# Performance work log

Measured on AMD Instinct MI355X. Metric: run time of the kernel, lower is better.

## Reference

```python
import jax, jax.numpy as jnp
import numpy as np

B, T, D, H = 8, 4096, 1024, 1024

def setup_inputs() -> dict:
    key = jax.random.key(0)
    k1, k2, k3, k4, k5 = jax.random.split(key, 5)
    s = 1.0 / np.sqrt(D)  # nn.Linear default init scale
    return {
        "x": jax.random.normal(k1, (B, T, D), dtype=jnp.float32),
        "Wz": jax.random.uniform(k2, (H, D), dtype=jnp.float32, minval=-s, maxval=s),
        "bz": jax.random.uniform(k3, (H,), dtype=jnp.float32, minval=-s, maxval=s),
        "Wh": jax.random.uniform(k4, (H, D), dtype=jnp.float32, minval=-s, maxval=s),
        "bh": jax.random.uniform(k5, (H,), dtype=jnp.float32, minval=-s, maxval=s),
    }

def log_g(x):
    # Appendix B.3 of 'Were RNNs All We Needed?'
    return jnp.where(x >= 0, jnp.log(jax.nn.relu(x) + 0.5), -jax.nn.softplus(-x))

def reference(x, Wz, bz, Wh, bh):
    # Linear projections: [B,T,D] @ [D,H] -> [B,T,H]
    k = jnp.einsum('btd,hd->bth', x, Wz) + bz
    tilde_h = jnp.einsum('btd,hd->bth', x, Wh) + bh
    log_z = -jax.nn.softplus(-k)           # log sigmoid(k)
    log_one_minus_z = -jax.nn.softplus(k)  # log (1 - sigmoid(k))
    log_tilde_h = log_g(tilde_h)
    # parallel scan in log space: h[i] = a[i]*h[i-1] + b[i]
    log_a_star = jnp.cumsum(log_one_minus_z, axis=1)
    log_x = log_a_star + jax.lax.cumlogsumexp(log_z + log_tilde_h - log_a_star, axis=1)
    return jnp.exp(log_x)
```

## Files before the change

kernel.cpp:

```cpp
#include <hip/hip_runtime.h>
#include <cstdint>

typedef unsigned short u16;
typedef __attribute__((ext_vector_type(8))) __bf16 bf16x8_t;
typedef __attribute__((ext_vector_type(4))) float f32x4_t;
typedef __attribute__((ext_vector_type(4))) _Float16 f16x4_t;

constexpr int Bn = 8, Tn = 4096, Dn = 1024, Hn = 1024;
constexpr int Mn = Bn * Tn;
constexpr int NC = 128, CL = Tn / NC;

__device__ __forceinline__ u16 f2bf(float f) {
  uint32_t u = __builtin_bit_cast(uint32_t, f);
  u += 0x7FFFu + ((u >> 16) & 1u);
  return (u16)(u >> 16);
}

__global__ __launch_bounds__(256) void cvt_bf16_kernel(const float* __restrict__ src,
                                                       u16* __restrict__ dst, int n4) {
  int i = blockIdx.x * 256 + threadIdx.x;
  if (i >= n4) return;
  float4 v = ((const float4*)src)[i];
  ushort4 o;
  o.x = f2bf(v.x); o.y = f2bf(v.y); o.z = f2bf(v.z); o.w = f2bf(v.w);
  ((ushort4*)dst)[i] = o;
}

__device__ __forceinline__ void gl_lds16(const void* g, void* l) {
  __builtin_amdgcn_global_load_lds((const __attribute__((address_space(1))) void*)g,
                                   (__attribute__((address_space(3))) void*)l, 16u, 0, 0u);
}

__global__ __launch_bounds__(256) void gemm_dual(
    const u16* __restrict__ A, const u16* __restrict__ Wz, const u16* __restrict__ Wh,
    const float* __restrict__ bz, const float* __restrict__ bh,
    u16* __restrict__ kout, u16* __restrict__ thout) {
  constexpr int K = 1024, N = 1024;
  const uint bid = blockIdx.x;
  const uint xcd = bid & 7;
  const uint seq = bid >> 3;
  uint nb = seq & 15;
  const uint mt = (seq >> 4) * 8 + xcd;
  const u16* Bm; const float* bias; u16* Cout;
  if (nb < N / 128) { Bm = Wz; bias = bz; Cout = kout; }
  else             { Bm = Wh; bias = bh; Cout = thout; nb -= N / 128; }
  const int m0 = mt * 128;
  const int n0 = nb * 128;

  __shared__ u16 lA[128 * 32];
  __shared__ u16 lB[128 * 32];

  const int tid  = threadIdx.x;
  const int lane = tid & 63;
  const int wave = tid >> 6;
  const int wm = (wave >> 1) * 64;
  const int wn = (wave & 1) * 64;

  f32x4_t acc[4][4] = {};

  const int e0 = (wave * 1024 + lane * 16) >> 1;
  const int r0 = e0 >> 5, c0 = e0 & 31;
  const u16* gA0 = A  + (size_t)(m0 + r0) * K + c0;
  const u16* gB0 = Bm + (size_t)(n0 + r0) * K + c0;
  u16* lAw = lA + wave * 512;
  u16* lBw = lB + wave * 512;

  const int fr = lane & 15;
  const int fk = (lane >> 4) * 8;

  for (int kt = 0; kt < K; kt += 32) {
    gl_lds16(gA0 + kt,           lAw);
    gl_lds16(gA0 + kt + 64 * K,  lAw + 2048);
    gl_lds16(gB0 + kt,           lBw);
    gl_lds16(gB0 + kt + 64 * K,  lBw + 2048);
    __syncthreads();
    bf16x8_t af[4], bfr[4];
#pragma unroll
    for (int i = 0; i < 4; ++i)
      af[i] = *(const bf16x8_t*)&lA[(wm + i * 16 + fr) * 32 + fk];
#pragma unroll
    for (int j = 0; j < 4; ++j)
      bfr[j] = *(const bf16x8_t*)&lB[(wn + j * 16 + fr) * 32 + fk];
#pragma unroll
    for (int i = 0; i < 4; ++i)
#pragma unroll
      for (int j = 0; j < 4; ++j)
        acc[i][j] = __builtin_amdgcn_mfma_f32_16x16x32_bf16(af[i], bfr[j], acc[i][j], 0, 0, 0);
    __syncthreads();
  }

  const int cr = (lane >> 4) * 4;
  const int cc = lane & 15;
#pragma unroll
  for (int j = 0; j < 4; ++j) {
    float bv = bias[n0 + wn + j * 16 + cc];
#pragma unroll
    for (int i = 0; i < 4; ++i) {
      u16* p = Cout + (size_t)(m0 + wm + i * 16 + cr) * N + (n0 + wn + j * 16 + cc);
#pragma unroll
      for (int r = 0; r < 4; ++r) {
        _Float16 hv = (_Float16)(acc[i][j][r] + bv);
        p[(size_t)r * N] = __builtin_bit_cast(u16, hv);
      }
    }
  }
}

__device__ __forceinline__ void gates(float kv, float tv, float& a, float& bb) {
  float e = __expf(-kv);
  float z = 1.f / (1.f + e);
  a = e * z;
  float g = (tv >= 0.f) ? (tv + 0.5f) : (1.f / (1.f + __expf(-tv)));
  bb = z * g;
}

__global__ __launch_bounds__(256) void scan_phase_a(
    const u16* __restrict__ kbuf, const u16* __restrict__ thbuf,
    float* __restrict__ Aagg, float* __restrict__ Bagg) {
  int h0 = threadIdx.x * 4;
  int c = blockIdx.x, b = blockIdx.y;
  size_t base = ((size_t)b * Tn + (size_t)c * CL) * Hn + h0;
  f32x4_t Aacc = {1.f, 1.f, 1.f, 1.f};
  f32x4_t Bacc = {};
#pragma unroll 4
  for (int t = 0; t < CL; ++t) {
    f16x4_t kv = *(const f16x4_t*)(kbuf + base + (size_t)t * Hn);
    f16x4_t tv = *(const f16x4_t*)(thbuf + base + (size_t)t * Hn);
#pragma unroll
    for (int u = 0; u < 4; ++u) {
      float a, bb;
      gates((float)kv[u], (float)tv[u], a, bb);
      Aacc[u] *= a;
      Bacc[u] = fmaf(a, Bacc[u], bb);
    }
  }
  size_t idx = ((size_t)b * NC + c) * Hn + h0;
  *(f32x4_t*)(Aagg + idx) = Aacc;
  *(f32x4_t*)(Bagg + idx) = Bacc;
}

__global__ __launch_bounds__(256) void scan_phase_b(
    const float* Aagg, const float* __restrict__ Bagg, float* carry) {
  int h = blockIdx.x * 256 + threadIdx.x;
  int b = blockIdx.y;
  float state = 0.f;
  for (int c = 0; c < NC; ++c) {
    size_t idx = ((size_t)b * NC + c) * Hn + h;
    float Av = Aagg[idx];
    float Bv = Bagg[idx];
    carry[idx] = state;
    state = fmaf(Av, state, Bv);
  }
}

__global__ __launch_bounds__(256) void scan_phase_c(
    const u16* __restrict__ kbuf, const u16* __restrict__ thbuf,
    const float* __restrict__ carry, float* __restrict__ out) {
  int h0 = threadIdx.x * 4;
  int c = blockIdx.x, b = blockIdx.y;
  f32x4_t hst = *(const f32x4_t*)(carry + ((size_t)b * NC + c) * Hn + h0);
  size_t base = ((size_t)b * Tn + (size_t)c * CL) * Hn + h0;
#pragma unroll 4
  for (int t = 0; t < CL; ++t) {
    size_t idx = base + (size_t)t * Hn;
    f16x4_t kv = *(const f16x4_t*)(kbuf + idx);
    f16x4_t tv = *(const f16x4_t*)(thbuf + idx);
#pragma unroll
    for (int u = 0; u < 4; ++u) {
      float a, bb;
      gates((float)kv[u], (float)tv[u], a, bb);
      hst[u] = fmaf(a, hst[u], bb);
    }
    *(f32x4_t*)(out + idx) = hst;
  }
}

extern "C" void kernel_launch(void* const* d_in, const int* in_sizes, int n_in,
                              void* d_out, int out_size, void* d_ws, size_t ws_size,
                              hipStream_t stream) {
  const float* x  = (const float*)d_in[0];
  const float* Wz = (const float*)d_in[1];
  const float* bz = (const float*)d_in[2];
  const float* Wh = (const float*)d_in[3];
  const float* bh = (const float*)d_in[4];
  float* out = (float*)d_out;

  char* ws = (char*)d_ws;
  u16*   xbf   = (u16*)  (ws);
  u16*   wzbf  = (u16*)  (ws + 67108864);
  u16*   whbf  = (u16*)  (ws + 69206016);
  u16*   kf16  = (u16*)  (ws + 71303168);
  u16*   thf16 = (u16*)  (ws + 138412032);
  float* Aagg  = (float*)(ws + 205520896);
  float* Bagg  = (float*)(ws + 209715200);
  float* carry = Aagg;

  cvt_bf16_kernel<<<dim3(Mn * Dn / 4 / 256), 256, 0, stream>>>(x,  xbf,  Mn * Dn / 4);
  cvt_bf16_kernel<<<dim3(Hn * Dn / 4 / 256), 256, 0, stream>>>(Wz, wzbf, Hn * Dn / 4);
  cvt_bf16_kernel<<<dim3(Hn * Dn / 4 / 256), 256, 0, stream>>>(Wh, whbf, Hn * Dn / 4);
  gemm_dual<<<dim3(4096), 256, 0, stream>>>(xbf, wzbf, whbf, bz, bh, kf16, thf16);
  scan_phase_a<<<dim3(NC, Bn), 256, 0, stream>>>(kf16, thf16, Aagg, Bagg);
  scan_phase_b<<<dim3(Hn / 256, Bn), 256, 0, stream>>>(Aagg, Bagg, carry);
  scan_phase_c<<<dim3(NC, Bn), 256, 0, stream>>>(kf16, thf16, carry, out);
}
```

Baseline: 502.3 us.

## Fuse gate computation and chunk-scan reduction into dual GEMM epilogue

The GEMM now computes both the Wz and Wh projections for the same 64-column H tile in one block and applies the gate nonlinearities in its epilogue. It writes packed fp16 (a,b) pairs and reduces each 32-row chunk into the Aagg/Bagg aggregates with wave shuffles, so the separate phase-A scan pass over k/tilde_h is gone. Phase C now reads precomputed gates instead of recomputing exponentials, the three conversion launches become one, and the LDS layout gets an XOR swizzle. The cost is more epilogue work in the GEMM, a smaller per-wave tile (32x64 times two), and gates rounded to fp16 before the scan.

Result: faster. 464.9 us (-7.4%).

```diff
diff --git a/kernel.cpp b/kernel.cpp
--- a/kernel.cpp
+++ b/kernel.cpp
@@ -4,7 +4,6 @@
 typedef unsigned short u16;
 typedef __attribute__((ext_vector_type(8))) __bf16 bf16x8_t;
 typedef __attribute__((ext_vector_type(4))) float f32x4_t;
-typedef __attribute__((ext_vector_type(4))) _Float16 f16x4_t;
 
 constexpr int Bn = 8, Tn = 4096, Dn = 1024, Hn = 1024;
 constexpr int Mn = Bn * Tn;
@@ -16,14 +15,18 @@
   return (u16)(u >> 16);
 }
 
-__global__ __launch_bounds__(256) void cvt_bf16_kernel(const float* __restrict__ src,
-                                                       u16* __restrict__ dst, int n4) {
+__global__ __launch_bounds__(256) void cvt_all(
+    const float* __restrict__ x, const float* __restrict__ wz, const float* __restrict__ wh,
+    u16* __restrict__ xb, u16* __restrict__ wzb, u16* __restrict__ whb) {
   int i = blockIdx.x * 256 + threadIdx.x;
-  if (i >= n4) return;
-  float4 v = ((const float4*)src)[i];
+  const float* s; u16* d; int off;
+  if (i < 8388608)      { s = x;  d = xb;  off = i; }
+  else if (i < 8650752) { s = wz; d = wzb; off = i - 8388608; }
+  else                  { s = wh; d = whb; off = i - 8650752; }
+  float4 v = ((const float4*)s)[off];
   ushort4 o;
   o.x = f2bf(v.x); o.y = f2bf(v.y); o.z = f2bf(v.z); o.w = f2bf(v.w);
-  ((ushort4*)dst)[i] = o;
+  ((ushort4*)d)[off] = o;
 }
 
 __device__ __forceinline__ void gl_lds16(const void* g, void* l) {
@@ -31,121 +34,126 @@
                                    (__attribute__((address_space(3))) void*)l, 16u, 0, 0u);
 }
 
-__global__ __launch_bounds__(256) void gemm_dual(
+__device__ __forceinline__ void gates(float kv, float tv, float& a, float& bb) {
+  float e  = __expf(-kv);
+  float rc = __builtin_amdgcn_rcpf(1.f + e);
+  a = e * rc;
+  float g = (tv >= 0.f) ? (tv + 0.5f)
+                        : __builtin_amdgcn_rcpf(1.f + __expf(-tv));
+  bb = rc * g;
+}
+
+__global__ __launch_bounds__(256) void gemm_fused(
     const u16* __restrict__ A, const u16* __restrict__ Wz, const u16* __restrict__ Wh,
     const float* __restrict__ bz, const float* __restrict__ bh,
-    u16* __restrict__ kout, u16* __restrict__ thout) {
-  constexpr int K = 1024, N = 1024;
+    uint32_t* __restrict__ gAB, float* __restrict__ Aagg, float* __restrict__ Bagg) {
+  constexpr int K = 1024;
   const uint bid = blockIdx.x;
   const uint xcd = bid & 7;
   const uint seq = bid >> 3;
-  uint nb = seq & 15;
-  const uint mt = (seq >> 4) * 8 + xcd;
-  const u16* Bm; const float* bias; u16* Cout;
-  if (nb < N / 128) { Bm = Wz; bias = bz; Cout = kout; }
-  else             { Bm = Wh; bias = bh; Cout = thout; nb -= N / 128; }
+  const uint ht  = seq & 15;
+  const uint mt  = (seq >> 4) * 8 + xcd;
   const int m0 = mt * 128;
-  const int n0 = nb * 128;
+  const int h0 = ht * 64;
 
   __shared__ u16 lA[128 * 32];
-  __shared__ u16 lB[128 * 32];
+  __shared__ u16 lB[2][64 * 32];
 
   const int tid  = threadIdx.x;
   const int lane = tid & 63;
   const int wave = tid >> 6;
-  const int wm = (wave >> 1) * 64;
-  const int wn = (wave & 1) * 64;
-
-  f32x4_t acc[4][4] = {};
-
-  const int e0 = (wave * 1024 + lane * 16) >> 1;
-  const int r0 = e0 >> 5, c0 = e0 & 31;
-  const u16* gA0 = A  + (size_t)(m0 + r0) * K + c0;
-  const u16* gB0 = Bm + (size_t)(n0 + r0) * K + c0;
-  u16* lAw = lA + wave * 512;
-  u16* lBw = lB + wave * 512;
-
-  const int fr = lane & 15;
-  const int fk = (lane >> 4) * 8;
+
+  const int csA = (((lane & 3) ^ ((lane >> 3) & 3)) * 8);
+  const int csB = (((tid  & 3) ^ ((tid  >> 3) & 3)) * 8);
+  const u16* gA0 = A  + (size_t)(m0 + wave * 16 + (lane >> 2)) * K + csA;
+  const u16* gBz = Wz + (size_t)(h0 + (tid >> 2)) * K + csB;
+  const u16* gBh = Wh + (size_t)(h0 + (tid >> 2)) * K + csB;
+  u16* lAw  = lA    + wave * 512;
+  u16* lBw0 = lB[0] + wave * 512;
+  u16* lBw1 = lB[1] + wave * 512;
+
+  const int fr   = lane & 15;
+  const int KB   = lane >> 4;
+  const int fcol = (KB ^ ((fr >> 1) & 3)) * 8;
+
+  f32x4_t az[2][4] = {}, ah[2][4] = {};
 
   for (int kt = 0; kt < K; kt += 32) {
-    gl_lds16(gA0 + kt,           lAw);
-    gl_lds16(gA0 + kt + 64 * K,  lAw + 2048);
-    gl_lds16(gB0 + kt,           lBw);
-    gl_lds16(gB0 + kt + 64 * K,  lBw + 2048);
+    gl_lds16(gA0 + kt,                    lAw);
+    gl_lds16(gA0 + kt + (size_t)64 * K,   lAw + 2048);
+    gl_lds16(gBz + kt,                    lBw0);
+    gl_lds16(gBh + kt,                    lBw1);
     __syncthreads();
-    bf16x8_t af[4], bfr[4];
-#pragma unroll
-    for (int i = 0; i < 4; ++i)
-      af[i] = *(const bf16x8_t*)&lA[(wm + i * 16 + fr) * 32 + fk];
-#pragma unroll
-    for (int j = 0; j < 4; ++j)
-      bfr[j] = *(const bf16x8_t*)&lB[(wn + j * 16 + fr) * 32 + fk];
-#pragma unroll
-    for (int i = 0; i < 4; ++i)
-#pragma unroll
-      for (int j = 0; j < 4; ++j)
-        acc[i][j] = __builtin_amdgcn_mfma_f32_16x16x32_bf16(af[i], bfr[j], acc[i][j], 0, 0, 0);
+    bf16x8_t af[2], bzf[4], bhf[4];
+#pragma unroll
+    for (int i = 0; i < 2; ++i)
+      af[i] = *(const bf16x8_t*)&lA[(wave * 32 + i * 16 + fr) * 32 + fcol];
+#pragma unroll
+    for (int j = 0; j < 4; ++j) {
+      bzf[j] = *(const bf16x8_t*)&lB[0][(j * 16 + fr) * 32 + fcol];
+      bhf[j] = *(const bf16x8_t*)&lB[1][(j * 16 + fr) * 32 + fcol];
+    }
+#pragma unroll
+    for (int i = 0; i < 2; ++i)
+#pragma unroll
+      for (int j = 0; j < 4; ++j) {
+        az[i][j] = __builtin_amdgcn_mfma_f32_16x16x32_bf16(af[i], bzf[j], az[i][j], 0, 0, 0);
+        ah[i][j] = __builtin_amdgcn_mfma_f32_16x16x32_bf16(af[i], bhf[j], ah[i][j], 0, 0, 0);
+      }
     __syncthreads();
   }
 
   const int cr = (lane >> 4) * 4;
   const int cc = lane & 15;
+  const int b  = mt >> 5;
+  const int tc = (mt & 31) * 4 + wave;
+
 #pragma unroll
   for (int j = 0; j < 4; ++j) {
-    float bv = bias[n0 + wn + j * 16 + cc];
-#pragma unroll
-    for (int i = 0; i < 4; ++i) {
-      u16* p = Cout + (size_t)(m0 + wm + i * 16 + cr) * N + (n0 + wn + j * 16 + cc);
+    float bvz = bz[h0 + j * 16 + cc];
+    float bvh = bh[h0 + j * 16 + cc];
+    float Ai[2], Bi[2];
+#pragma unroll
+    for (int i = 0; i < 2; ++i) {
+      float Al = 1.f, Bl = 0.f;
 #pragma unroll
       for (int r = 0; r < 4; ++r) {
-        _Float16 hv = (_Float16)(acc[i][j][r] + bv);
-        p[(size_t)r * N] = __builtin_bit_cast(u16, hv);
+        float kv = az[i][j][r] + bvz;
+        float tv = ah[i][j][r] + bvh;
+        float a, bb;
+        gates(kv, tv, a, bb);
+        _Float16 a16 = (_Float16)a, b16 = (_Float16)bb;
+        uint32_t pk = (uint32_t)__builtin_bit_cast(u16, a16) |
+                      ((uint32_t)__builtin_bit_cast(u16, b16) << 16);
+        gAB[(size_t)(m0 + wave * 32 + i * 16 + cr + r) * Hn + h0 + j * 16 + cc] = pk;
+        float ar = (float)a16, br = (float)b16;
+        Al = Al * ar;
+        Bl = fmaf(ar, Bl, br);
       }
-    }
-  }
-}
-
-__device__ __forceinline__ void gates(float kv, float tv, float& a, float& bb) {
-  float e = __expf(-kv);
-  float z = 1.f / (1.f + e);
-  a = e * z;
-  float g = (tv >= 0.f) ? (tv + 0.5f) : (1.f / (1.f + __expf(-tv)));
-  bb = z * g;
-}
-
-__global__ __launch_bounds__(256) void scan_phase_a(
-    const u16* __restrict__ kbuf, const u16* __restrict__ thbuf,
-    float* __restrict__ Aagg, float* __restrict__ Bagg) {
-  int h0 = threadIdx.x * 4;
-  int c = blockIdx.x, b = blockIdx.y;
-  size_t base = ((size_t)b * Tn + (size_t)c * CL) * Hn + h0;
-  f32x4_t Aacc = {1.f, 1.f, 1.f, 1.f};
-  f32x4_t Bacc = {};
-#pragma unroll 4
-  for (int t = 0; t < CL; ++t) {
-    f16x4_t kv = *(const f16x4_t*)(kbuf + base + (size_t)t * Hn);
-    f16x4_t tv = *(const f16x4_t*)(thbuf + base + (size_t)t * Hn);
-#pragma unroll
-    for (int u = 0; u < 4; ++u) {
-      float a, bb;
-      gates((float)kv[u], (float)tv[u], a, bb);
-      Aacc[u] *= a;
-      Bacc[u] = fmaf(a, Bacc[u], bb);
-    }
-  }
-  size_t idx = ((size_t)b * NC + c) * Hn + h0;
-  *(f32x4_t*)(Aagg + idx) = Aacc;
-  *(f32x4_t*)(Bagg + idx) = Bacc;
-}
-
-__global__ __launch_bounds__(256) void scan_phase_b(
+      float Ahi = __shfl_down(Al, 16), Bhi = __shfl_down(Bl, 16);
+      float A2 = Ahi * Al;
+      float B2 = fmaf(Ahi, Bl, Bhi);
+      Ahi = __shfl_down(A2, 32); Bhi = __shfl_down(B2, 32);
+      Ai[i] = Ahi * A2;
+      Bi[i] = fmaf(Ahi, B2, Bhi);
+    }
+    float Aw = Ai[1] * Ai[0];
+    float Bw = fmaf(Ai[1], Bi[0], Bi[1]);
+    if (lane < 16) {
+      size_t ai = ((size_t)(b * NC + tc)) * Hn + h0 + j * 16 + lane;
+      Aagg[ai] = Aw;
+      Bagg[ai] = Bw;
+    }
+  }
+}
+
+__global__ __launch_bounds__(64) void scan_phase_b(
     const float* Aagg, const float* __restrict__ Bagg, float* carry) {
-  int h = blockIdx.x * 256 + threadIdx.x;
+  int h = blockIdx.x * 64 + threadIdx.x;
   int b = blockIdx.y;
   float state = 0.f;
   for (int c = 0; c < NC; ++c) {
-    size_t idx = ((size_t)b * NC + c) * Hn + h;
+    size_t idx = ((size_t)(b * NC + c)) * Hn + h;
     float Av = Aagg[idx];
     float Bv = Bagg[idx];
     carry[idx] = state;
@@ -154,21 +162,21 @@
 }
 
 __global__ __launch_bounds__(256) void scan_phase_c(
-    const u16* __restrict__ kbuf, const u16* __restrict__ thbuf,
-    const float* __restrict__ carry, float* __restrict__ out) {
+    const uint32_t* __restrict__ gAB, const float* __restrict__ carry,
+    float* __restrict__ out) {
   int h0 = threadIdx.x * 4;
   int c = blockIdx.x, b = blockIdx.y;
-  f32x4_t hst = *(const f32x4_t*)(carry + ((size_t)b * NC + c) * Hn + h0);
+  f32x4_t hst = *(const f32x4_t*)(carry + ((size_t)(b * NC + c)) * Hn + h0);
   size_t base = ((size_t)b * Tn + (size_t)c * CL) * Hn + h0;
 #pragma unroll 4
   for (int t = 0; t < CL; ++t) {
     size_t idx = base + (size_t)t * Hn;
-    f16x4_t kv = *(const f16x4_t*)(kbuf + idx);
-    f16x4_t tv = *(const f16x4_t*)(thbuf + idx);
+    uint4 v = *(const uint4*)(gAB + idx);
+    uint32_t vv[4] = {v.x, v.y, v.z, v.w};
 #pragma unroll
     for (int u = 0; u < 4; ++u) {
-      float a, bb;
-      gates((float)kv[u], (float)tv[u], a, bb);
+      float a = (float)__builtin_bit_cast(_Float16, (u16)(vv[u] & 0xFFFFu));
+      float bb = (float)__builtin_bit_cast(_Float16, (u16)(vv[u] >> 16));
       hst[u] = fmaf(a, hst[u], bb);
     }
     *(f32x4_t*)(out + idx) = hst;
@@ -186,20 +194,16 @@
   float* out = (float*)d_out;
 
   char* ws = (char*)d_ws;
-  u16*   xbf   = (u16*)  (ws);
-  u16*   wzbf  = (u16*)  (ws + 67108864);
-  u16*   whbf  = (u16*)  (ws + 69206016);
-  u16*   kf16  = (u16*)  (ws + 71303168);
-  u16*   thf16 = (u16*)  (ws + 138412032);
-  float* Aagg  = (float*)(ws + 205520896);
-  float* Bagg  = (float*)(ws + 209715200);
-  float* carry = Aagg;
-
-  cvt_bf16_kernel<<<dim3(Mn * Dn / 4 / 256), 256, 0, stream>>>(x,  xbf,  Mn * Dn / 4);
-  cvt_bf16_kernel<<<dim3(Hn * Dn / 4 / 256), 256, 0, stream>>>(Wz, wzbf, Hn * Dn / 4);
-  cvt_bf16_kernel<<<dim3(Hn * Dn / 4 / 256), 256, 0, stream>>>(Wh, whbf, Hn * Dn / 4);
-  gemm_dual<<<dim3(4096), 256, 0, stream>>>(xbf, wzbf, whbf, bz, bh, kf16, thf16);
-  scan_phase_a<<<dim3(NC, Bn), 256, 0, stream>>>(kf16, thf16, Aagg, Bagg);
-  scan_phase_b<<<dim3(Hn / 256, Bn), 256, 0, stream>>>(Aagg, Bagg, carry);
-  scan_phase_c<<<dim3(NC, Bn), 256, 0, stream>>>(kf16, thf16, carry, out);
-}
+  u16*      xbf   = (u16*)     (ws);
+  u16*      wzbf  = (u16*)     (ws + 67108864);
+  u16*      whbf  = (u16*)     (ws + 69206016);
+  uint32_t* gAB   = (uint32_t*)(ws + 71303168);
+  float*    Aagg  = (float*)   (ws + 205520896);
+  float*    Bagg  = (float*)   (ws + 209715200);
+  float*    carry = Aagg;
+
+  cvt_all<<<dim3(34816), 256, 0, stream>>>(x, Wz, Wh, xbf, wzbf, whbf);
+  gemm_fused<<<dim3(4096), 256, 0, stream>>>(xbf, wzbf, whbf, bz, bh, gAB, Aagg, Bagg);
+  scan_phase_b<<<dim3(16, Bn), 64, 0, stream>>>(Aagg, Bagg, carry);
+  scan_phase_c<<<dim3(NC, Bn), 256, 0, stream>>>(gAB, carry, out);
+}
```
